# Kernel tuning notes

Measured on AMD Instinct MI355X. Metric: run time of the kernel, lower is better.

Reference implementation:

```python
import jax, jax.numpy as jnp
import numpy as np
from jax import lax


def _forward(matrix_states, candidate_actions, candidate_actions_features,
             conv_w, conv_b, wq, bq, wk, bk, wv, bv, wo, bo,
             mlp_w1, mlp_b1, mlp_w2, mlp_b2):
    # --- CNN feature extractor on each state matrix (batched, not looped) ---
    x = matrix_states[:, None, :, :]  # [M,1,H,W]
    c = lax.conv_general_dilated(
        x, conv_w, window_strides=(1, 1), padding=[(1, 1), (1, 1)],
        dimension_numbers=('NCHW', 'OIHW', 'NCHW'))
    c = jax.nn.relu(c + conv_b[None, :, None, None])  # [M,16,H+1,W+1]
    M, C, Hc, Wc = c.shape
    # AdaptiveAvgPool2d((2,2)) with even spatial dims -> exact half bins
    pooled = c.reshape(M, C, 2, Hc // 2, 2, Wc // 2).mean(axis=(3, 5))  # [M,16,2,2]
    state_feature = pooled.reshape(1, M * C * 4)  # torch cat of [1,64] feats -> [1, M*64]

    # --- gather candidate action features ---
    af = candidate_actions_features[candidate_actions]  # [A,F]
    A, F = af.shape

    # --- single-head self-attention over actions ---
    Q = af @ wq + bq  # [A,F]
    K = af @ wk + bk
    V = af @ wv + bv
    energy = (Q @ K.T) / jnp.sqrt(jnp.asarray(F, af.dtype))  # [A,A]
    attn = jax.nn.softmax(energy, axis=-1)
    out = attn @ V          # [A,F]
    out = out @ wo + bo     # fc_out

    # --- MLP scoring: concat(state_feature, action_feat) per action, batched ---
    st = jnp.broadcast_to(state_feature, (A, state_feature.shape[1]))  # [A,S]
    combined = jnp.concatenate([st, out], axis=1)  # [A, S+F]
    h = jax.nn.relu(combined @ mlp_w1 + mlp_b1)    # [A,16]
    scores = (h @ mlp_w2 + mlp_b2)[:, 0]           # [A]
    return jax.nn.softmax(scores, axis=0)


def setup_inputs() -> dict:
    key = jax.random.key(0)
    ks = jax.random.split(key, 12)
    M, H, W = 3, 255, 255
    A, Vtab, F = 8192, 16384, 16
    S = M * 64                # state feature dim = 192
    Dc = S + F                # combined_dim = 208
    f32 = jnp.float32

    def n(k, shape, scale):
        return jax.random.normal(k, shape, dtype=f32) * scale

    return {
        'matrix_states': jax.random.normal(ks[0], (M, H, W), dtype=f32),
        'candidate_actions': jax.random.randint(ks[1], (A,), 0, Vtab),
        'candidate_actions_features': jax.random.normal(ks[2], (Vtab, F), dtype=f32),
        'conv_w': n(ks[3], (16, 1, 2, 2), 0.5),
        'conv_b': jnp.zeros((16,), f32),
        'wq': n(ks[4], (F, F), 0.25), 'bq': jnp.zeros((F,), f32),
        'wk': n(ks[5], (F, F), 0.25), 'bk': jnp.zeros((F,), f32),
        'wv': n(ks[6], (F, F), 0.25), 'bv': jnp.zeros((F,), f32),
        'wo': n(ks[7], (F, F), 0.25), 'bo': jnp.zeros((F,), f32),
        'mlp_w1': n(ks[8], (Dc, 16), 0.07), 'mlp_b1': jnp.zeros((16,), f32),
        'mlp_w2': n(ks[9], (16, 1), 0.25), 'mlp_b2': jnp.zeros((1,), f32),
    }


def reference(matrix_states, candidate_actions, candidate_actions_features,
              conv_w, conv_b, wq, bq, wk, bk, wv, bv, wo, bo,
              mlp_w1, mlp_b1, mlp_w2, mlp_b2):
    return _forward(matrix_states, candidate_actions, candidate_actions_features,
                    conv_w, conv_b, wq, bq, wk, bk, wv, bv, wo, bo,
                    mlp_w1, mlp_b1, mlp_w2, mlp_b2)
```

## Files before the change

### kernel.cpp

```cpp
#include <hip/hip_runtime.h>
#include <hip/hip_bf16.h>

#define A_N 8192
#define LOG2E 1.44269504f

typedef __attribute__((ext_vector_type(8))) short short8v;
typedef __attribute__((ext_vector_type(4))) float f32x4;
typedef __attribute__((ext_vector_type(4))) int   i32x4;

__device__ inline short f2bf(float x) {
  unsigned u = __builtin_bit_cast(unsigned, x);
  unsigned r = (u + 0x7FFFu + ((u >> 16) & 1u)) >> 16;
  return (short)r;
}
__device__ inline float fexp2(float x) {
#if __has_builtin(__builtin_amdgcn_exp2f)
  return __builtin_amdgcn_exp2f(x);
#else
  return exp2f(x);
#endif
}
__device__ inline unsigned cvtpk2(float lo, float hi) {
  float2 t; t.x = lo; t.y = hi;
  __hip_bfloat162 h = __float22bfloat162_rn(t);
  unsigned r; __builtin_memcpy(&r, &h, 4);
  return r;
}

__global__ __launch_bounds__(256) void fused_pre(
    const float* __restrict__ x, const float* __restrict__ cw,
    const float* __restrict__ cb, float* __restrict__ sfp,
    const int* __restrict__ act, const float* __restrict__ feat,
    const float* __restrict__ wq, const float* __restrict__ bq,
    const float* __restrict__ wk, const float* __restrict__ bk,
    const float* __restrict__ wv, const float* __restrict__ bv,
    const float* __restrict__ wo,
    short* __restrict__ Qo, short* __restrict__ Ko, short* __restrict__ V2S,
    int* __restrict__ counter) {
  __shared__ float swq[256], swk[256], swv[256], swo[256];
  __shared__ float sbq[16], sbk[16], sbv[16];
  __shared__ float red[4];
  int tid = threadIdx.x;
  if (blockIdx.x == 0 && tid == 0) *counter = 0;
  if (blockIdx.x < 1536) {
    int bid2 = blockIdx.x;
    int u    = bid2 & 7;
    int base = bid2 >> 3;
    int b  = base & 1;
    int a  = (base >> 1) & 1;
    int ch = (base >> 2) & 15;
    int m  = base >> 6;
    float w00 = cw[ch*4+0], w01 = cw[ch*4+1], w10 = cw[ch*4+2], w11 = cw[ch*4+3];
    float bias = cb[ch];
    const float* xm = x + (size_t)m * 255 * 255;
    float sum = 0.f;
    #pragma unroll
    for (int it = 0; it < 8; ++it) {
      int p = u*2048 + it*256 + tid;
      int i = a*128 + (p >> 7);
      int j = b*128 + (p & 127);
      float x00 = (i >= 1 && j >= 1)   ? xm[(i-1)*255 + (j-1)] : 0.f;
      float x01 = (i >= 1 && j <= 254) ? xm[(i-1)*255 + j]     : 0.f;
      float x10 = (i <= 254 && j >= 1) ? xm[i*255 + (j-1)]     : 0.f;
      float x11 = (i <= 254 && j <= 254) ? xm[i*255 + j]       : 0.f;
      float v = fmaf(x00,w00, fmaf(x01,w01, fmaf(x10,w10, fmaf(x11,w11, bias))));
      sum += fmaxf(v, 0.f);
    }
    for (int o = 32; o; o >>= 1) sum += __shfl_down(sum, o, 64);
    int wid = tid >> 6, lane = tid & 63;
    if (lane == 0) red[wid] = sum;
    __syncthreads();
    if (tid == 0) sfp[bid2] = red[0]+red[1]+red[2]+red[3];
  } else {
    swq[tid] = wq[tid]; swk[tid] = wk[tid]; swv[tid] = wv[tid]; swo[tid] = wo[tid];
    if (tid < 16) { sbq[tid] = bq[tid]; sbk[tid] = bk[tid]; sbv[tid] = bv[tid]; }
    __syncthreads();
    int row = (blockIdx.x - 1536) * 256 + tid;
    int idx = act[row];
    const float4* f4 = (const float4*)(feat + (size_t)idx * 16);
    float4 a0 = f4[0], a1 = f4[1], a2 = f4[2], a3 = f4[3];
    float af[16] = {a0.x,a0.y,a0.z,a0.w, a1.x,a1.y,a1.z,a1.w,
                    a2.x,a2.y,a2.z,a2.w, a3.x,a3.y,a3.z,a3.w};
    float q[16], k[16], v[16];
    #pragma unroll
    for (int kk = 0; kk < 16; ++kk) {
      float aq = sbq[kk], ak = sbk[kk], av = sbv[kk];
      #pragma unroll
      for (int f = 0; f < 16; ++f) {
        aq = fmaf(af[f], swq[f*16+kk], aq);
        ak = fmaf(af[f], swk[f*16+kk], ak);
        av = fmaf(af[f], swv[f*16+kk], av);
      }
      q[kk] = aq; k[kk] = ak; v[kk] = av;
    }
    const float qs = 0.25f * LOG2E;
    int s  = row >> 5;
    int jj = row & 31;
    int hi = jj >> 4;
    int m2 = jj & 15;
    int gsw = m2 >> 2;
    int rsw = m2 & 3;
    size_t vbase = (size_t)s * 512 + (size_t)gsw * 128 + hi * 4 + rsw;
    #pragma unroll
    for (int kk = 0; kk < 16; ++kk) {
      float a = 0.f;
      #pragma unroll
      for (int f = 0; f < 16; ++f) a = fmaf(v[f], swo[f*16+kk], a);
      V2S[vbase + (size_t)kk * 8] = f2bf(a);
      Qo[(size_t)row*16 + kk] = f2bf(q[kk] * qs);
      Ko[(size_t)row*16 + kk] = f2bf(k[kk]);
    }
  }
}

__global__ __launch_bounds__(1024, 1) void attn_score(
    const short* __restrict__ Qb, const short* __restrict__ Kb,
    const short* __restrict__ V2S, const float* __restrict__ sfp,
    const float* __restrict__ w1, const float* __restrict__ b1,
    const float* __restrict__ bo, const float* __restrict__ w2,
    float* __restrict__ scores, int* __restrict__ counter,
    float* __restrict__ outp) {
  __shared__ float sacc[16][32][16];
  __shared__ float sl[16][32];
  __shared__ float sw1[256];
  __shared__ float scvp[16][16];
  __shared__ float scv[16], sw2s[16];
  __shared__ float red2[16];
  __shared__ float sbc2[2];
  __shared__ int slastS;
  int tid = threadIdx.x;
  if (tid < 256) {
    sw1[tid] = w1[192*16 + tid];
    int c4 = tid >> 4, kq = tid & 15;
    float acc = (c4 == 0) ? b1[kq] : 0.f;
    #pragma unroll
    for (int si = 0; si < 12; ++si) {
      int s = c4*12 + si;
      const float* pp = sfp + s*8;
      float sv = ((pp[0]+pp[1])+(pp[2]+pp[3])) + ((pp[4]+pp[5])+(pp[6]+pp[7]));
      acc = fmaf(sv * (1.0f/16384.0f), w1[s*16+kq], acc);
    }
    if (c4 == 1) {
      #pragma unroll
      for (int f = 0; f < 16; ++f) acc = fmaf(bo[f], w1[(192+f)*16+kq], acc);
    }
    scvp[c4][kq] = acc;
  }
  if (tid < 16) sw2s[tid] = w2[tid];
  int w = tid >> 6, lane = tid & 63;
  int g = lane >> 4, fi = lane & 15;
  int i0 = blockIdx.x * 32;

  short8v z8 = {};
  short8v qfa = z8, qfb = z8;
  if (g < 2) {
    qfa = *(const short8v*)(Qb + (size_t)(i0 + fi)*16 + g*8);
    qfb = *(const short8v*)(Qb + (size_t)(i0 + 16 + fi)*16 + g*8);
  }
  const short* kp = Kb + (size_t)(w*512 + fi)*16 + g*8;
  const short* vp = V2S + (size_t)(w*1024 + lane)*8;

  f32x4 acca = {0.f,0.f,0.f,0.f}, accb = {0.f,0.f,0.f,0.f};
  float lsa = 0.f, lsb = 0.f;

  short8v k0c = *(const short8v*)kp;
  short8v k1c = *(const short8v*)(kp + 256);
  i32x4  vvc = *(const i32x4*)(vp);
  short8v k0x = *(const short8v*)(kp + 512);
  short8v k1x = *(const short8v*)(kp + 768);
  i32x4  vvx = *(const i32x4*)(vp + 512);

  #pragma unroll
  for (int step = 0; step < 16; ++step) {
    short8v k0n = z8, k1n = z8; i32x4 vvn = {0,0,0,0};
    if (step < 14) {
      k0n = *(const short8v*)(kp + 1024);
      k1n = *(const short8v*)(kp + 1280);
      vvn = *(const i32x4*)(vp + 1024);
    }
    short8v vf = __builtin_bit_cast(short8v, vvc);
    f32x4 zero4 = {0.f,0.f,0.f,0.f};
    f32x4 e0a = __builtin_amdgcn_mfma_f32_16x16x32_bf16(k0c, qfa, zero4, 0, 0, 0);
    f32x4 e1a = __builtin_amdgcn_mfma_f32_16x16x32_bf16(k1c, qfa, zero4, 0, 0, 0);
    f32x4 e0b = __builtin_amdgcn_mfma_f32_16x16x32_bf16(k0c, qfb, zero4, 0, 0, 0);
    f32x4 e1b = __builtin_amdgcn_mfma_f32_16x16x32_bf16(k1c, qfb, zero4, 0, 0, 0);
    {
      float p0 = fexp2(e0a[0]), p1 = fexp2(e0a[1]), p2 = fexp2(e0a[2]), p3 = fexp2(e0a[3]);
      float p4 = fexp2(e1a[0]), p5 = fexp2(e1a[1]), p6 = fexp2(e1a[2]), p7 = fexp2(e1a[3]);
      lsa += ((p0+p1)+(p2+p3)) + ((p4+p5)+(p6+p7));
      i32x4 pk;
      pk[0] = (int)cvtpk2(p0, p1); pk[1] = (int)cvtpk2(p2, p3);
      pk[2] = (int)cvtpk2(p4, p5); pk[3] = (int)cvtpk2(p6, p7);
      acca = __builtin_amdgcn_mfma_f32_16x16x32_bf16(__builtin_bit_cast(short8v, pk), vf, acca, 0, 0, 0);
    }
    {
      float p0 = fexp2(e0b[0]), p1 = fexp2(e0b[1]), p2 = fexp2(e0b[2]), p3 = fexp2(e0b[3]);
      float p4 = fexp2(e1b[0]), p5 = fexp2(e1b[1]), p6 = fexp2(e1b[2]), p7 = fexp2(e1b[3]);
      lsb += ((p0+p1)+(p2+p3)) + ((p4+p5)+(p6+p7));
      i32x4 pk;
      pk[0] = (int)cvtpk2(p0, p1); pk[1] = (int)cvtpk2(p2, p3);
      pk[2] = (int)cvtpk2(p4, p5); pk[3] = (int)cvtpk2(p6, p7);
      accb = __builtin_amdgcn_mfma_f32_16x16x32_bf16(__builtin_bit_cast(short8v, pk), vf, accb, 0, 0, 0);
    }
    k0c = k0x; k1c = k1x; vvc = vvx;
    k0x = k0n; k1x = k1n; vvx = vvn;
    kp += 512;
    vp += 512;
  }
  lsa += __shfl_xor(lsa, 16, 64); lsa += __shfl_xor(lsa, 32, 64);
  lsb += __shfl_xor(lsb, 16, 64); lsb += __shfl_xor(lsb, 32, 64);
  #pragma unroll
  for (int r = 0; r < 4; ++r) {
    sacc[w][4*g + r][fi]      = acca[r];
    sacc[w][16 + 4*g + r][fi] = accb[r];
  }
  if (g == 0) { sl[w][fi] = lsa; sl[w][16 + fi] = lsb; }
  __syncthreads();
  if (tid < 512) {
    int i = tid >> 4, f = tid & 15;
    float o = 0.f, li = 0.f;
    #pragma unroll
    for (int wv = 0; wv < 16; ++wv) { o += sacc[wv][i][f]; li += sl[wv][i]; }
    sacc[0][i][f] = o / li;
  } else if (tid < 528) {
    int k = tid - 512;
    float s = 0.f;
    #pragma unroll
    for (int c = 0; c < 16; ++c) s += scvp[c][k];
    scv[k] = s;
  }
  __syncthreads();
  if (tid < 512) {
    int i = tid >> 4, k = tid & 15;
    float h = scv[k];
    #pragma unroll
    for (int f = 0; f < 16; ++f) h = fmaf(sacc[0][i][f], sw1[f*16+k], h);
    h = fmaxf(h, 0.f);
    float t = h * sw2s[k];
    t += __shfl_xor(t, 1, 64);
    t += __shfl_xor(t, 2, 64);
    t += __shfl_xor(t, 4, 64);
    t += __shfl_xor(t, 8, 64);
    if (k == 0)
      __hip_atomic_store(&scores[i0 + i], t, __ATOMIC_RELAXED, __HIP_MEMORY_SCOPE_AGENT);
  }
  __syncthreads();
  if (tid == 0)
    slastS = __hip_atomic_fetch_add(counter, 1, __ATOMIC_ACQ_REL, __HIP_MEMORY_SCOPE_AGENT);
  __syncthreads();
  if (slastS != (A_N/32) - 1) return;

  float sv[8];
  #pragma unroll
  for (int u = 0; u < 8; ++u)
    sv[u] = __hip_atomic_load(&scores[tid + u*1024], __ATOMIC_RELAXED, __HIP_MEMORY_SCOPE_AGENT);
  int lane2 = tid & 63, wid2 = tid >> 6;
  float m = -3.4e38f;
  #pragma unroll
  for (int u = 0; u < 8; ++u) m = fmaxf(m, sv[u]);
  for (int o = 32; o; o >>= 1) m = fmaxf(m, __shfl_down(m, o, 64));
  if (lane2 == 0) red2[wid2] = m;
  __syncthreads();
  if (tid == 0) {
    float mm = red2[0];
    for (int wv = 1; wv < 16; ++wv) mm = fmaxf(mm, red2[wv]);
    sbc2[0] = mm;
  }
  __syncthreads();
  float mx = sbc2[0];
  float s = 0.f;
  #pragma unroll
  for (int u = 0; u < 8; ++u) s += __expf(sv[u] - mx);
  for (int o = 32; o; o >>= 1) s += __shfl_down(s, o, 64);
  if (lane2 == 0) red2[wid2] = s;
  __syncthreads();
  if (tid == 0) {
    float ss = 0.f;
    for (int wv = 0; wv < 16; ++wv) ss += red2[wv];
    sbc2[1] = ss;
  }
  __syncthreads();
  float inv = 1.0f / sbc2[1];
  #pragma unroll
  for (int u = 0; u < 8; ++u)
    outp[tid + u*1024] = __expf(sv[u] - mx) * inv;
}

extern "C" void kernel_launch(void* const* d_in, const int* in_sizes, int n_in,
                              void* d_out, int out_size, void* d_ws, size_t ws_size,
                              hipStream_t stream) {
  const float* x      = (const float*)d_in[0];
  const int*   act    = (const int*)  d_in[1];
  const float* feat   = (const float*)d_in[2];
  const float* conv_w = (const float*)d_in[3];
  const float* conv_b = (const float*)d_in[4];
  const float* wq     = (const float*)d_in[5];
  const float* bq     = (const float*)d_in[6];
  const float* wk     = (const float*)d_in[7];
  const float* bk     = (const float*)d_in[8];
  const float* wv     = (const float*)d_in[9];
  const float* bv     = (const float*)d_in[10];
  const float* wo     = (const float*)d_in[11];
  const float* bo     = (const float*)d_in[12];
  const float* w1     = (const float*)d_in[13];
  const float* b1     = (const float*)d_in[14];
  const float* w2     = (const float*)d_in[15];

  char* wsb = (char*)d_ws;
  float* sfp    = (float*)(wsb);
  int*   ctr    = (int*)  (wsb + 8192);
  float* scores = (float*)(wsb + 16384);
  short* Qb     = (short*)(wsb + 65536);
  short* Kb     = (short*)(wsb + 65536 + 262144);
  short* V2S    = (short*)(wsb + 65536 + 524288);
  float* out    = (float*)d_out;

  fused_pre  <<<1568, 256, 0, stream>>>(x, conv_w, conv_b, sfp,
                                        act, feat, wq, bq, wk, bk, wv, bv, wo,
                                        Qb, Kb, V2S, ctr);
  attn_score <<<A_N/32, 1024, 0, stream>>>(Qb, Kb, V2S, sfp, w1, b1, bo, w2,
                                           scores, ctr, out);
}
```

Before: 35.10 us.

## Use 16x16x16 MFMA for QK^T with repacked K layout and single K load

```diff
diff --git a/kernel.cpp b/kernel.cpp
--- a/kernel.cpp
+++ b/kernel.cpp
@@ -5,6 +5,7 @@
 #define LOG2E 1.44269504f
 
 typedef __attribute__((ext_vector_type(8))) short short8v;
+typedef __attribute__((ext_vector_type(4))) short short4v;
 typedef __attribute__((ext_vector_type(4))) float f32x4;
 typedef __attribute__((ext_vector_type(4))) int   i32x4;
 
@@ -42,8 +43,8 @@
   __shared__ float red[4];
   int tid = threadIdx.x;
   if (blockIdx.x == 0 && tid == 0) *counter = 0;
-  if (blockIdx.x < 1536) {
-    int bid2 = blockIdx.x;
+  if (blockIdx.x >= 32) {
+    int bid2 = blockIdx.x - 32;
     int u    = bid2 & 7;
     int base = bid2 >> 3;
     int b  = base & 1;
@@ -75,7 +76,7 @@
     swq[tid] = wq[tid]; swk[tid] = wk[tid]; swv[tid] = wv[tid]; swo[tid] = wo[tid];
     if (tid < 16) { sbq[tid] = bq[tid]; sbk[tid] = bk[tid]; sbv[tid] = bv[tid]; }
     __syncthreads();
-    int row = (blockIdx.x - 1536) * 256 + tid;
+    int row = blockIdx.x * 256 + tid;
     int idx = act[row];
     const float4* f4 = (const float4*)(feat + (size_t)idx * 16);
     float4 a0 = f4[0], a1 = f4[1], a2 = f4[2], a3 = f4[3];
@@ -101,6 +102,7 @@
     int gsw = m2 >> 2;
     int rsw = m2 & 3;
     size_t vbase = (size_t)s * 512 + (size_t)gsw * 128 + hi * 4 + rsw;
+    size_t kbase = (size_t)s * 512 + (size_t)m2 * 8 + (size_t)hi * 4;
     #pragma unroll
     for (int kk = 0; kk < 16; ++kk) {
       float a = 0.f;
@@ -108,7 +110,7 @@
       for (int f = 0; f < 16; ++f) a = fmaf(v[f], swo[f*16+kk], a);
       V2S[vbase + (size_t)kk * 8] = f2bf(a);
       Qo[(size_t)row*16 + kk] = f2bf(q[kk] * qs);
-      Ko[(size_t)row*16 + kk] = f2bf(k[kk]);
+      Ko[kbase + (size_t)(kk >> 2) * 128 + (kk & 3)] = f2bf(k[kk]);
     }
   }
 }
@@ -151,39 +153,35 @@
   int g = lane >> 4, fi = lane & 15;
   int i0 = blockIdx.x * 32;
 
-  short8v z8 = {};
-  short8v qfa = z8, qfb = z8;
-  if (g < 2) {
-    qfa = *(const short8v*)(Qb + (size_t)(i0 + fi)*16 + g*8);
-    qfb = *(const short8v*)(Qb + (size_t)(i0 + 16 + fi)*16 + g*8);
-  }
-  const short* kp = Kb + (size_t)(w*512 + fi)*16 + g*8;
+  short4v qfa = *(const short4v*)(Qb + (size_t)(i0 + fi)*16 + g*4);
+  short4v qfb = *(const short4v*)(Qb + (size_t)(i0 + 16 + fi)*16 + g*4);
+  const short* kp = Kb + (size_t)w*8192 + (size_t)lane*8;
   const short* vp = V2S + (size_t)(w*1024 + lane)*8;
 
   f32x4 acca = {0.f,0.f,0.f,0.f}, accb = {0.f,0.f,0.f,0.f};
   float lsa = 0.f, lsb = 0.f;
 
-  short8v k0c = *(const short8v*)kp;
-  short8v k1c = *(const short8v*)(kp + 256);
-  i32x4  vvc = *(const i32x4*)(vp);
-  short8v k0x = *(const short8v*)(kp + 512);
-  short8v k1x = *(const short8v*)(kp + 768);
-  i32x4  vvx = *(const i32x4*)(vp + 512);
+  i32x4 kvc = *(const i32x4*)(kp);
+  i32x4 vvc = *(const i32x4*)(vp);
+  i32x4 kvx = *(const i32x4*)(kp + 512);
+  i32x4 vvx = *(const i32x4*)(vp + 512);
 
   #pragma unroll
   for (int step = 0; step < 16; ++step) {
-    short8v k0n = z8, k1n = z8; i32x4 vvn = {0,0,0,0};
+    i32x4 kvn = {0,0,0,0}, vvn = {0,0,0,0};
     if (step < 14) {
-      k0n = *(const short8v*)(kp + 1024);
-      k1n = *(const short8v*)(kp + 1280);
+      kvn = *(const i32x4*)(kp + 1024);
       vvn = *(const i32x4*)(vp + 1024);
     }
+    short8v kw = __builtin_bit_cast(short8v, kvc);
+    short4v k0c = {kw[0], kw[1], kw[2], kw[3]};
+    short4v k1c = {kw[4], kw[5], kw[6], kw[7]};
     short8v vf = __builtin_bit_cast(short8v, vvc);
     f32x4 zero4 = {0.f,0.f,0.f,0.f};
-    f32x4 e0a = __builtin_amdgcn_mfma_f32_16x16x32_bf16(k0c, qfa, zero4, 0, 0, 0);
-    f32x4 e1a = __builtin_amdgcn_mfma_f32_16x16x32_bf16(k1c, qfa, zero4, 0, 0, 0);
-    f32x4 e0b = __builtin_amdgcn_mfma_f32_16x16x32_bf16(k0c, qfb, zero4, 0, 0, 0);
-    f32x4 e1b = __builtin_amdgcn_mfma_f32_16x16x32_bf16(k1c, qfb, zero4, 0, 0, 0);
+    f32x4 e0a = __builtin_amdgcn_mfma_f32_16x16x16bf16_1k(k0c, qfa, zero4, 0, 0, 0);
+    f32x4 e1a = __builtin_amdgcn_mfma_f32_16x16x16bf16_1k(k1c, qfa, zero4, 0, 0, 0);
+    f32x4 e0b = __builtin_amdgcn_mfma_f32_16x16x16bf16_1k(k0c, qfb, zero4, 0, 0, 0);
+    f32x4 e1b = __builtin_amdgcn_mfma_f32_16x16x16bf16_1k(k1c, qfb, zero4, 0, 0, 0);
     {
       float p0 = fexp2(e0a[0]), p1 = fexp2(e0a[1]), p2 = fexp2(e0a[2]), p3 = fexp2(e0a[3]);
       float p4 = fexp2(e1a[0]), p5 = fexp2(e1a[1]), p6 = fexp2(e1a[2]), p7 = fexp2(e1a[3]);
@@ -202,8 +200,8 @@
       pk[2] = (int)cvtpk2(p4, p5); pk[3] = (int)cvtpk2(p6, p7);
       accb = __builtin_amdgcn_mfma_f32_16x16x32_bf16(__builtin_bit_cast(short8v, pk), vf, accb, 0, 0, 0);
     }
-    k0c = k0x; k1c = k1x; vvc = vvx;
-    k0x = k0n; k1x = k1n; vvx = vvn;
+    kvc = kvx; vvc = vvx;
+    kvx = kvn; vvx = vvn;
     kp += 512;
     vp += 512;
   }
```

Result: faster. 31.96 us (-9.0%).
